# Optimization experiments

Measured on AMD Instinct MI355X. Metric: run time of the kernel, lower is better.

## Reference

```python
import jax, jax.numpy as jnp
import numpy as np

DATA = 2048   # data_size / hidden_size
WIDTH = 4096  # width_size
T = 1000      # len(ts)


def setup_inputs() -> dict:
    key = jax.random.key(0)
    ks = jax.random.split(key, 10)
    # ts: evenly spaced times; small dt keeps 1000 Euler steps stable
    ts = jnp.arange(T, dtype=jnp.float32) * 1e-3
    y0 = jax.random.normal(ks[0], (DATA,), dtype=jnp.float32)
    def lin(k, fan_out, fan_in):
        kw, kb = jax.random.split(k)
        s = 1.0 / np.sqrt(fan_in)
        W = jax.random.uniform(kw, (fan_out, fan_in), jnp.float32, -s, s)
        b = jax.random.uniform(kb, (fan_out,), jnp.float32, -s, s)
        return W, b
    # eqx.nn.MLP(depth=3): in->w, w->w, w->w, w->out, softplus on all but last
    W0, b0 = lin(ks[1], WIDTH, DATA)
    W1, b1 = lin(ks[2], WIDTH, WIDTH)
    W2, b2 = lin(ks[3], WIDTH, WIDTH)
    W3, b3 = lin(ks[4], DATA, WIDTH)
    return {"ts": ts, "y0": y0, "W0": W0, "b0": b0, "W1": W1, "b1": b1,
            "W2": W2, "b2": b2, "W3": W3, "b3": b3}


def reference(ts, y0, W0, b0, W1, b1, W2, b2, W3, b3):
    dt = ts[1] - ts[0]

    def mlp(y):
        h = jax.nn.softplus(W0 @ y + b0)
        h = jax.nn.softplus(W1 @ h + b1)
        h = jax.nn.softplus(W2 @ h + b2)
        return W3 @ h + b3

    def step(y, _):
        y1 = y + dt * mlp(y)  # Euler step: y + dt * f(t, y)
        return y1, y1

    _, ys = jax.lax.scan(step, y0, None, length=ts.shape[0])
    return ys  # [T, DATA]
```

## Files before the change

### kernel.cpp

```cpp
#include <hip/hip_runtime.h>

#define NWG   256
#define TPB_R 256
#define TPB_S 1024
#define NSTEP 1000
#define NDATA 2048
#define WIDTH 4096

typedef __attribute__((ext_vector_type(4))) float f32x4;
typedef __attribute__((ext_vector_type(2))) float f32x2;
typedef __attribute__((ext_vector_type(2))) unsigned int u32x2;
typedef __attribute__((ext_vector_type(4))) unsigned int u32x4;
typedef unsigned int uint;

#define SCHED_FENCE() __builtin_amdgcn_sched_barrier(0)


__device__ __forceinline__ float sp_f(float v) {
  return fmaxf(v, 0.0f) + log1pf(expf(-fabsf(v)));
}

__device__ __forceinline__ float wred(float v) {
#pragma unroll
  for (int m = 32; m > 0; m >>= 1) v += __shfl_xor(v, m, 64);
  return v;
}

__device__ __forceinline__ uint pk_bf16(float lo, float hi) {
  uint r;
  asm("v_cvt_pk_bf16_f32 %0, %1, %2" : "=v"(r) : "v"(lo), "v"(hi));
  return r;
}


__device__ __forceinline__ void wait_vm0()   { asm volatile("s_waitcnt vmcnt(0)" ::: "memory"); SCHED_FENCE(); }
template<int N>
__device__ __forceinline__ void wait_vmN()   { asm volatile("s_waitcnt vmcnt(%0)" :: "n"(N) : "memory"); SCHED_FENCE(); }
__device__ __forceinline__ void wait_lgkm0() { asm volatile("s_waitcnt lgkmcnt(0)" ::: "memory"); SCHED_FENCE(); }
__device__ __forceinline__ void wgbar()      { __builtin_amdgcn_s_barrier(); SCHED_FENCE(); }


__device__ __forceinline__ void st_sc_x1(float* p, float v) {
  asm volatile("global_store_dword %0, %1, off sc0 sc1" :: "v"(p), "v"(v) : "memory");
}
__device__ __forceinline__ void st_sc_x2(float* p, f32x2 v) {
  asm volatile("global_store_dwordx2 %0, %1, off sc0 sc1" :: "v"(p), "v"(v) : "memory");
}
__device__ __forceinline__ void st_sc_u2(uint* p, u32x2 v) {
  asm volatile("global_store_dwordx2 %0, %1, off sc0 sc1" :: "v"(p), "v"(v) : "memory");
}
__device__ __forceinline__ void ld_sc_x2_issue(const float* p, f32x2& v) {
  asm volatile("global_load_dwordx2 %0, %1, off sc0 sc1" : "=v"(v) : "v"(p) : "memory");
}
__device__ __forceinline__ void ld_sc_x4_issue(const f32x4* p, f32x4& v) {
  asm volatile("global_load_dwordx4 %0, %1, off sc0 sc1" : "=v"(v) : "v"(p) : "memory");
}
__device__ __forceinline__ void ld_sc_u4_issue(const u32x4* p, u32x4& v) {
  asm volatile("global_load_dwordx4 %0, %1, off sc0 sc1" : "=v"(v) : "v"(p) : "memory");
}
__device__ __forceinline__ void ld_sc_x1_issue(const float* p, float& v) {
  asm volatile("global_load_dword %0, %1, off sc0 sc1" : "=v"(v) : "v"(p) : "memory");
}
__device__ __forceinline__ uint ld_sc_u32(const uint* p) {
  uint v;
  asm volatile("global_load_dword %0, %1, off sc0 sc1\n\ts_waitcnt vmcnt(0)"
               : "=v"(v) : "v"(p) : "memory");
  return v;
}
__device__ __forceinline__ void st_sc_u32(uint* p, uint v) {
  asm volatile("global_store_dword %0, %1, off sc0 sc1" :: "v"(p), "v"(v) : "memory");
}

__device__ __forceinline__ void ld_g(const u32x4* p, u32x4& v) {
  asm volatile("global_load_dwordx4 %0, %1, off" : "=v"(v) : "v"(p) : "memory");
}


__device__ __forceinline__ void sync_stage_h(uint* flags, uint tag, int wg,
                                             int tid, const uint* src,
                                             uint* xs) {
  wgbar();
  if (tid == 0) st_sc_u32(flags + wg * 16, tag);
  const uint* fp = flags + tid * 16;
  if (ld_sc_u32(fp) < tag) {
    do { __builtin_amdgcn_s_sleep(1); } while (ld_sc_u32(fp) < tag);
  }
  const u32x4* s = (const u32x4*)src + tid * 2;
  u32x4 a, b;
  ld_sc_u4_issue(s + 0, a); ld_sc_u4_issue(s + 1, b);
  wait_vm0();
  u32x4* l = (u32x4*)xs + tid * 2;
  l[0] = a; l[1] = b;
  wait_lgkm0();
  wgbar();
}

__device__ __forceinline__ void sync_stage_y(uint* flags, uint tag, int wg,
                                             int tid, const float* src,
                                             uint* xs) {
  wgbar();
  if (tid == 0) st_sc_u32(flags + wg * 16, tag);
  const uint* fp = flags + tid * 16;
  if (ld_sc_u32(fp) < tag) {
    do { __builtin_amdgcn_s_sleep(1); } while (ld_sc_u32(fp) < tag);
  }
  const f32x4* s = (const f32x4*)src + tid * 2;
  f32x4 a, b;
  ld_sc_x4_issue(s + 0, a); ld_sc_x4_issue(s + 1, b);
  wait_vm0();
  u32x4 o;
  o.x = pk_bf16(a.x, a.y); o.y = pk_bf16(a.z, a.w);
  o.z = pk_bf16(b.x, b.y); o.w = pk_bf16(b.z, b.w);
  ((u32x4*)xs)[tid] = o;
  wait_lgkm0();
  wgbar();
}


__device__ __forceinline__ uint bfr(float f) {
  uint u = __float_as_uint(f);
  return (u + 0x7fffu + ((u >> 16) & 1u)) >> 16;
}

__global__ void cvt_perm(const float* __restrict__ in, u32x4* __restrict__ out,
                         int rows, int K) {
  int idx = blockIdx.x * 256 + threadIdx.x;
  int cpr = K >> 3;
  if (idx >= rows * cpr) return;
  int row = idx / cpr, c = idx - row * cpr;
  int j = c >> 6, lane = c & 63;
  const f32x4* p = (const f32x4*)(in + (size_t)row * K + j * 512 + lane * 4);
  f32x4 lo = p[0];
  f32x4 hi = p[64];
  u32x4 o;
  o.x = bfr(lo.x) | (bfr(lo.y) << 16);
  o.y = bfr(lo.z) | (bfr(lo.w) << 16);
  o.z = bfr(hi.x) | (bfr(hi.y) << 16);
  o.w = bfr(hi.z) | (bfr(hi.w) << 16);
  out[idx] = o;
}


#define VD(W, X, s) asm("v_dot2_f32_bf16 %0, %1, %2, %0" : "+v"(s) : "v"(W), "v"(X))

#define QF(Q, s) do{                                                 \
  VD((Q).x, xa2.x, s); VD((Q).y, xa2.y, s);                          \
  VD((Q).z, xb2.x, s); VD((Q).w, xb2.y, s);                          \
}while(0)

#define DC(Q, j, s) do{                                              \
  u32x2 xa2 = xw2[(j)*128 + lane];                                   \
  u32x2 xb2 = xw2[(j)*128 + 64 + lane];                              \
  QF(Q, s);                                                          \
}while(0)

#define DL4(j) do{                                                   \
  u32x2 xa2 = xw2[(j)*128 + lane];                                   \
  u32x2 xb2 = xw2[(j)*128 + 64 + lane];                              \
  u32x4 Q0 = w1p[0*512 + (j)*64 + lane];                             \
  u32x4 Q1 = w1p[1*512 + (j)*64 + lane];                             \
  u32x4 Q2 = w1p[2*512 + (j)*64 + lane];                             \
  u32x4 Q3 = w1p[3*512 + (j)*64 + lane];                             \
  QF(Q0, s0); QF(Q1, s1); QF(Q2, s2); QF(Q3, s3);                    \
}while(0)

#define DR4(j, Qa, Qb, Qc, Qd) do{                                   \
  u32x2 xa2 = xw2[(j)*128 + lane];                                   \
  u32x2 xb2 = xw2[(j)*128 + 64 + lane];                              \
  QF(Qa, s0); QF(Qb, s1); QF(Qc, s2); QF(Qd, s3);                    \
}while(0)

#define DR2(j, Qa, Qb) do{                                           \
  u32x2 xa2 = xw2[(j)*128 + lane];                                   \
  u32x2 xb2 = xw2[(j)*128 + 64 + lane];                              \
  QF(Qa, s0); QF(Qb, s1);                                            \
}while(0)

#define SREG(x) __int_as_float(__builtin_amdgcn_readfirstlane(__float_as_int(x)))


__global__ void __launch_bounds__(TPB_R, 1) ode_res(
    const float* __restrict__ ts, const float* __restrict__ y0,
    const u32x4* __restrict__ W0p, const float* __restrict__ b0,
    const u32x4* __restrict__ W1p, const float* __restrict__ b1,
    const u32x4* __restrict__ W2p, const float* __restrict__ b2,
    const u32x4* __restrict__ W3p, const float* __restrict__ b3,
    float* __restrict__ out, uint* hA, uint* hB,
    uint* flags)
{
  __shared__ u32x4 W1lds[16 * 512];
  __shared__ uint xs[2048];
  const int wg = blockIdx.x, tid = threadIdx.x;
  const int wave = tid >> 6, lane = tid & 63;
  const float dt = ts[1] - ts[0];
  const int rw = wg * 16 + wave * 4;
  const int rf = wg * 8 + wave * 2;
  const u32x2* xw2 = (const u32x2*)xs;
  const u32x4* w1p = &W1lds[(wave * 4) * 512];

#pragma unroll
  for (int k = 0; k < 32; ++k)
    W1lds[k * 256 + tid] = W1p[(size_t)wg * 8192 + k * 256 + tid];

#define L2W(r,j) W2p[(size_t)(rw+(r))*512 + (j)*64 + lane]
  u32x4 C00=L2W(0,0),C01=L2W(0,1),C02=L2W(0,2),C03=L2W(0,3),C04=L2W(0,4),C05=L2W(0,5),C06=L2W(0,6),C07=L2W(0,7);
  u32x4 C10=L2W(1,0),C11=L2W(1,1),C12=L2W(1,2),C13=L2W(1,3),C14=L2W(1,4),C15=L2W(1,5),C16=L2W(1,6),C17=L2W(1,7);
  u32x4 C20=L2W(2,0),C21=L2W(2,1),C22=L2W(2,2),C23=L2W(2,3),C24=L2W(2,4),C25=L2W(2,5),C26=L2W(2,6),C27=L2W(2,7);
  u32x4 C30=L2W(3,0),C31=L2W(3,1),C32=L2W(3,2),C33=L2W(3,3),C34=L2W(3,4),C35=L2W(3,5),C36=L2W(3,6),C37=L2W(3,7);
#define L3W(r,j) W3p[(size_t)(rf+(r))*512 + (j)*64 + lane]
  u32x4 D00=L3W(0,0),D01=L3W(0,1),D02=L3W(0,2),D03=L3W(0,3),D04=L3W(0,4),D05=L3W(0,5),D06=L3W(0,6),D07=L3W(0,7);
  u32x4 D10=L3W(1,0),D11=L3W(1,1),D12=L3W(1,2),D13=L3W(1,3),D14=L3W(1,4),D15=L3W(1,5),D16=L3W(1,6),D17=L3W(1,7);

  const float b00=SREG(b0[rw]), b01=SREG(b0[rw+1]), b02=SREG(b0[rw+2]), b03=SREG(b0[rw+3]);
  const float b10=SREG(b1[rw]), b11=SREG(b1[rw+1]), b12=SREG(b1[rw+2]), b13=SREG(b1[rw+3]);
  const float b20=SREG(b2[rw]), b21=SREG(b2[rw+1]), b22=SREG(b2[rw+2]), b23=SREG(b2[rw+3]);
  const float b30=SREG(b3[rf]), b31=SREG(b3[rf+1]);

  wait_vm0(); wait_lgkm0();
  wgbar();

  const u32x4* w0base = W0p + (size_t)rw * 256 + lane;
#define ISSW0(r, Qa, Qb, Qc, Qd) do{ const u32x4* p_ = w0base + (size_t)(r)*256; \
  ld_g(p_, Qa); ld_g(p_+64, Qb); ld_g(p_+128, Qc); ld_g(p_+192, Qd); }while(0)

  u32x4 E0a,E0b,E0c,E0d, E1a,E1b,E1c,E1d, E2a,E2b,E2c,E2d, E3a,E3b,E3c,E3d;
  ISSW0(0, E0a,E0b,E0c,E0d);

  uint tag = 0;
  const float* yin = y0;
  for (int step = 0; step < NSTEP; ++step) {
    float s0, s1, s2, s3;
    sync_stage_y(flags, tag, wg, tid, yin, xs); ++tag;
    ISSW0(1, E1a,E1b,E1c,E1d);
    s0 = 0.f; DC(E0a,0,s0); DC(E0b,1,s0); DC(E0c,2,s0); DC(E0d,3,s0);
    ISSW0(2, E2a,E2b,E2c,E2d);
    wait_vmN<4>();
    s1 = 0.f; DC(E1a,0,s1); DC(E1b,1,s1); DC(E1c,2,s1); DC(E1d,3,s1);
    ISSW0(3, E3a,E3b,E3c,E3d);
    wait_vmN<4>();
    s2 = 0.f; DC(E2a,0,s2); DC(E2b,1,s2); DC(E2c,2,s2); DC(E2d,3,s2);
    wait_vm0();
    s3 = 0.f; DC(E3a,0,s3); DC(E3b,1,s3); DC(E3c,2,s3); DC(E3d,3,s3);
    s0 = wred(s0); s1 = wred(s1); s2 = wred(s2); s3 = wred(s3);
    if (lane == 0) {
      u32x2 v; v.x = pk_bf16(sp_f(s0+b00), sp_f(s1+b01));
               v.y = pk_bf16(sp_f(s2+b02), sp_f(s3+b03));
      st_sc_u2(hA + (rw >> 1), v);
    }
    wait_vm0();

    sync_stage_h(flags, tag, wg, tid, hA, xs); ++tag;
    s0=0.f; s1=0.f; s2=0.f; s3=0.f;
    DL4(0); DL4(1); DL4(2); DL4(3); DL4(4); DL4(5); DL4(6); DL4(7);
    s0 = wred(s0); s1 = wred(s1); s2 = wred(s2); s3 = wred(s3);
    if (lane == 0) {
      u32x2 v; v.x = pk_bf16(sp_f(s0+b10), sp_f(s1+b11));
               v.y = pk_bf16(sp_f(s2+b12), sp_f(s3+b13));
      st_sc_u2(hB + (rw >> 1), v);
    }
    wait_vm0();

    sync_stage_h(flags, tag, wg, tid, hB, xs); ++tag;
    s0=0.f; s1=0.f; s2=0.f; s3=0.f;
    DR4(0, C00, C10, C20, C30); DR4(1, C01, C11, C21, C31);
    DR4(2, C02, C12, C22, C32); DR4(3, C03, C13, C23, C33);
    DR4(4, C04, C14, C24, C34); DR4(5, C05, C15, C25, C35);
    DR4(6, C06, C16, C26, C36); DR4(7, C07, C17, C27, C37);
    s0 = wred(s0); s1 = wred(s1); s2 = wred(s2); s3 = wred(s3);
    if (lane == 0) {
      u32x2 v; v.x = pk_bf16(sp_f(s0+b20), sp_f(s1+b21));
               v.y = pk_bf16(sp_f(s2+b22), sp_f(s3+b23));
      st_sc_u2(hA + (rw >> 1), v);
    }
    wait_vm0();

    sync_stage_h(flags, tag, wg, tid, hA, xs); ++tag;
    f32x2 yo;
    ld_sc_x2_issue(yin + rf, yo);
    s0=0.f; s1=0.f;
    DR2(0, D00, D10); DR2(1, D01, D11); DR2(2, D02, D12); DR2(3, D03, D13);
    DR2(4, D04, D14); DR2(5, D05, D15); DR2(6, D06, D16); DR2(7, D07, D17);
    s0 = wred(s0); s1 = wred(s1);
    wait_vm0();
    float* yout = out + (size_t)step * NDATA;
    if (lane == 0) {
      f32x2 v; v.x = yo.x + dt * (s0 + b30); v.y = yo.y + dt * (s1 + b31);
      st_sc_x2(yout + rf, v);
    }
    ISSW0(0, E0a,E0b,E0c,E0d);
    wait_vmN<4>();
    yin = yout;
  }
}


__device__ __forceinline__ void gbar1k(uint* flags, uint tag, int wg, int tid) {
  wgbar();
  if (tid == 0) st_sc_u32(flags + wg * 16, tag);
  if (tid < NWG) {
    const uint* fp = flags + tid * 16;
    if (ld_sc_u32(fp) < tag) {
      do { __builtin_amdgcn_s_sleep(1); } while (ld_sc_u32(fp) < tag);
    }
  }
  wgbar();
}

__device__ __forceinline__ void stage4096_1k(const float* src, float* xs, int tid) {
  f32x4 a;
  ld_sc_x4_issue((const f32x4*)src + tid, a);
  wait_vm0();
  ((f32x4*)xs)[tid] = a;
  wait_lgkm0();
  wgbar();
}
__device__ __forceinline__ void stage2048_1k(const float* src, float* xs, int tid) {
  f32x4 a;
  bool act = tid < 512;
  if (act) ld_sc_x4_issue((const f32x4*)src + tid, a);
  wait_vm0();
  if (act) ((f32x4*)xs)[tid] = a;
  wait_lgkm0();
  wgbar();
}

__device__ __forceinline__ void issue_row_f32(const float* W, size_t elemidx, int lane, f32x4* wr, int ni) {
  const f32x4* p = (const f32x4*)(W + elemidx) + lane;
  for (int i = 0; i < ni; ++i)
    asm volatile("global_load_dwordx4 %0, %1, off" : "=v"(wr[i]) : "v"(p + i * 64) : "memory");
}

template<int NI>
__device__ __forceinline__ float dot_row_f32(const f32x4* wr, const float* xs, int xoff, int lane) {
  const f32x4* x4 = (const f32x4*)xs + xoff;
  float a = 0.f;
#pragma unroll
  for (int i = 0; i < NI; ++i) {
    f32x4 xv = x4[i * 64 + lane];
    a = fmaf(wr[i].x, xv.x, a); a = fmaf(wr[i].y, xv.y, a);
    a = fmaf(wr[i].z, xv.z, a); a = fmaf(wr[i].w, xv.w, a);
  }
  return a;
}

__global__ void __launch_bounds__(TPB_S, 1) ode_stream(
    const float* __restrict__ ts, const float* __restrict__ y0,
    const float* __restrict__ W0, const float* __restrict__ b0,
    const float* __restrict__ W1, const float* __restrict__ b1,
    const float* __restrict__ W2, const float* __restrict__ b2,
    const float* __restrict__ W3, const float* __restrict__ b3,
    float* __restrict__ out, float* hA, float* hB,
    uint* flags)
{
  __shared__ float xs[WIDTH];
  __shared__ float ps[16];
  const int wg = blockIdx.x, tid = threadIdx.x;
  const int wave = tid >> 6, lane = tid & 63;
  const float dt = ts[1] - ts[0];
  const int rw = wg * 16 + wave;
  const int rF = wg * 8 + (wave >> 1);
  const int hf = wave & 1;

  f32x4 w0r[8], w1r[16], w2r[16], w3r[8];
  issue_row_f32(W0, (size_t)rw * NDATA, lane, w0r, 8);

  uint tag = 0;
  const float* yin = y0;
  for (int step = 0; step < NSTEP; ++step) {
    stage2048_1k(yin, xs, tid);
    float a = wred(dot_row_f32<8>(w0r, xs, 0, lane));
    if (lane == 0) st_sc_x1(hA + rw, sp_f(a + b0[rw]));
    issue_row_f32(W1, (size_t)rw * WIDTH, lane, w1r, 16);
    wait_vmN<16>();
    gbar1k(flags, ++tag, wg, tid);

    stage4096_1k(hA, xs, tid);
    a = wred(dot_row_f32<16>(w1r, xs, 0, lane));
    if (lane == 0) st_sc_x1(hB + rw, sp_f(a + b1[rw]));
    issue_row_f32(W2, (size_t)rw * WIDTH, lane, w2r, 16);
    wait_vmN<16>();
    gbar1k(flags, ++tag, wg, tid);

    stage4096_1k(hB, xs, tid);
    a = wred(dot_row_f32<16>(w2r, xs, 0, lane));
    if (lane == 0) st_sc_x1(hA + rw, sp_f(a + b2[rw]));
    issue_row_f32(W3, (size_t)rF * WIDTH + (size_t)hf * 2048, lane, w3r, 8);
    wait_vmN<8>();
    gbar1k(flags, ++tag, wg, tid);

    stage4096_1k(hA, xs, tid);
    float yo;
    ld_sc_x1_issue(yin + rF, yo);
    a = wred(dot_row_f32<8>(w3r, xs, hf * 512, lane));
    if (lane == 0) ps[wave] = a;
    wait_lgkm0();
    wgbar();
    wait_vm0();
    float* yout = out + (size_t)step * NDATA;
    if (hf == 0 && lane == 0) {
      float tot = ps[wave] + ps[wave + 1];
      st_sc_x1(yout + rF, yo + dt * (tot + b3[rF]));
    }
    issue_row_f32(W0, (size_t)rw * NDATA, lane, w0r, 8);
    wait_vmN<8>();
    gbar1k(flags, ++tag, wg, tid);
    yin = yout;
  }
}


#define WS_HA   0
#define WS_HB   16384
#define WS_CNT  32768
#define WS_WB   65536
static const size_t N_W0 = (size_t)WIDTH * NDATA;
static const size_t N_W1 = (size_t)WIDTH * WIDTH;
static const size_t N_W3 = (size_t)NDATA * WIDTH;

extern "C" void kernel_launch(void* const* d_in, const int* in_sizes, int n_in,
                              void* d_out, int out_size, void* d_ws, size_t ws_size,
                              hipStream_t stream) {
  const float* ts = (const float*)d_in[0];
  const float* y0 = (const float*)d_in[1];
  const float* W0 = (const float*)d_in[2];
  const float* b0 = (const float*)d_in[3];
  const float* W1 = (const float*)d_in[4];
  const float* b1 = (const float*)d_in[5];
  const float* W2 = (const float*)d_in[6];
  const float* b2 = (const float*)d_in[7];
  const float* W3 = (const float*)d_in[8];
  const float* b3 = (const float*)d_in[9];
  float* out = (float*)d_out;

  char* ws = (char*)d_ws;
  uint*  flags = (uint*)(ws + WS_CNT);

  hipMemsetAsync(ws + WS_CNT, 0, 16384, stream);

  const size_t need = WS_WB + (N_W0 + 2 * N_W1 + N_W3) * 2;
  if (ws_size >= need) {
    u32x4* W0p = (u32x4*)(ws + WS_WB);
    u32x4* W1p = W0p + N_W0 / 8;
    u32x4* W2p = W1p + N_W1 / 8;
    u32x4* W3p = W2p + N_W1 / 8;
    uint* hA = (uint*)(ws + WS_HA);
    uint* hB = (uint*)(ws + WS_HB);
    hipLaunchKernelGGL(cvt_perm, dim3((unsigned)(N_W0 / 8 / 256)), dim3(256), 0, stream, W0, W0p, WIDTH, NDATA);
    hipLaunchKernelGGL(cvt_perm, dim3((unsigned)(N_W1 / 8 / 256)), dim3(256), 0, stream, W1, W1p, WIDTH, WIDTH);
    hipLaunchKernelGGL(cvt_perm, dim3((unsigned)(N_W1 / 8 / 256)), dim3(256), 0, stream, W2, W2p, WIDTH, WIDTH);
    hipLaunchKernelGGL(cvt_perm, dim3((unsigned)(N_W3 / 8 / 256)), dim3(256), 0, stream, W3, W3p, NDATA, WIDTH);
    hipLaunchKernelGGL(ode_res, dim3(NWG), dim3(TPB_R), 0, stream,
                       ts, y0, W0p, b0, W1p, b1, W2p, b2, W3p, b3,
                       out, hA, hB, flags);
  } else {
    float* hAf = (float*)(ws + WS_HA);
    float* hBf = (float*)(ws + WS_HB);
    hipLaunchKernelGGL(ode_stream, dim3(NWG), dim3(TPB_S), 0, stream,
                       ts, y0, W0, b0, W1, b1, W2, b2, W3, b3,
                       out, hAf, hBf, flags);
  }
}
```

Baseline: 19.87 ms.

## Fold W3 and next-step W0 into precomputed G matrix to drop one grid barrier per step

Precomputes G = W0·W3 with a one-time GEMM kernel. Each Euler step then updates the first-layer pre-activation directly as u += dt·(G·h2 + W0·b3), while y is still computed from W3 for output. This removes one of the four grid-wide syncs per step and fuses the y→layer0 dependency. In exchange it streams an extra 4096x4096 bf16 matrix from global memory every step, adds a setup GEMM, and lets the pre-activation accumulate rounding drift relative to recomputing from y.

```diff
diff --git a/kernel.cpp b/kernel.cpp
--- a/kernel.cpp
+++ b/kernel.cpp
@@ -70,7 +70,6 @@
 __device__ __forceinline__ void st_sc_u32(uint* p, uint v) {
   asm volatile("global_store_dword %0, %1, off sc0 sc1" :: "v"(p), "v"(v) : "memory");
 }
-
 __device__ __forceinline__ void ld_g(const u32x4* p, u32x4& v) {
   asm volatile("global_load_dwordx4 %0, %1, off" : "=v"(v) : "v"(p) : "memory");
 }
@@ -108,6 +107,18 @@
   f32x4 a, b;
   ld_sc_x4_issue(s + 0, a); ld_sc_x4_issue(s + 1, b);
   wait_vm0();
+  u32x4 o;
+  o.x = pk_bf16(a.x, a.y); o.y = pk_bf16(a.z, a.w);
+  o.z = pk_bf16(b.x, b.y); o.w = pk_bf16(b.z, b.w);
+  ((u32x4*)xs)[tid] = o;
+  wait_lgkm0();
+  wgbar();
+}
+
+__device__ __forceinline__ void stage_plain_2048(const float* src, uint* xs, int tid) {
+  wgbar();
+  const f32x4* s = (const f32x4*)src + tid * 2;
+  f32x4 a = s[0], b = s[1];
   u32x4 o;
   o.x = pk_bf16(a.x, a.y); o.y = pk_bf16(a.z, a.w);
   o.z = pk_bf16(b.x, b.y); o.w = pk_bf16(b.z, b.w);
@@ -141,6 +152,63 @@
 }
 
 
+__global__ void __launch_bounds__(256) gemm_G(const float* __restrict__ W0,
+                                              const float* __restrict__ W3,
+                                              uint* __restrict__ Gp) {
+  __shared__ float As[64][33];
+  __shared__ float Bs[32][65];
+  const int bid = blockIdx.x;
+  const int tr = bid >> 6, tc = bid & 63;
+  const int r0 = tr * 64, c0 = tc * 64;
+  const int tid = threadIdx.x;
+  float acc[4][4] = {};
+  for (int kb = 0; kb < 2048; kb += 32) {
+    {
+      int row = tid >> 2, kk = (tid & 3) * 8;
+      const float* src = W0 + (size_t)(r0 + row) * 2048 + kb + kk;
+#pragma unroll
+      for (int i = 0; i < 8; ++i) As[row][kk + i] = src[i];
+    }
+    {
+      int k = tid >> 3, cc = (tid & 7) * 8;
+      const float* src = W3 + (size_t)(kb + k) * 4096 + c0 + cc;
+#pragma unroll
+      for (int i = 0; i < 8; ++i) Bs[k][cc + i] = src[i];
+    }
+    __syncthreads();
+    const int rr = (tid >> 4) * 4, cc = (tid & 15) * 4;
+#pragma unroll
+    for (int k = 0; k < 32; ++k) {
+      float a0 = As[rr + 0][k], a1 = As[rr + 1][k], a2 = As[rr + 2][k], a3 = As[rr + 3][k];
+      float bx0 = Bs[k][cc + 0], bx1 = Bs[k][cc + 1], bx2 = Bs[k][cc + 2], bx3 = Bs[k][cc + 3];
+      acc[0][0] = fmaf(a0, bx0, acc[0][0]); acc[0][1] = fmaf(a0, bx1, acc[0][1]);
+      acc[0][2] = fmaf(a0, bx2, acc[0][2]); acc[0][3] = fmaf(a0, bx3, acc[0][3]);
+      acc[1][0] = fmaf(a1, bx0, acc[1][0]); acc[1][1] = fmaf(a1, bx1, acc[1][1]);
+      acc[1][2] = fmaf(a1, bx2, acc[1][2]); acc[1][3] = fmaf(a1, bx3, acc[1][3]);
+      acc[2][0] = fmaf(a2, bx0, acc[2][0]); acc[2][1] = fmaf(a2, bx1, acc[2][1]);
+      acc[2][2] = fmaf(a2, bx2, acc[2][2]); acc[2][3] = fmaf(a2, bx3, acc[2][3]);
+      acc[3][0] = fmaf(a3, bx0, acc[3][0]); acc[3][1] = fmaf(a3, bx1, acc[3][1]);
+      acc[3][2] = fmaf(a3, bx2, acc[3][2]); acc[3][3] = fmaf(a3, bx3, acc[3][3]);
+    }
+    __syncthreads();
+  }
+  const int rr = (tid >> 4) * 4, cc = (tid & 15) * 4;
+#pragma unroll
+  for (int i = 0; i < 4; ++i) {
+    int r = r0 + rr + i;
+    int c = c0 + cc;
+    int j = c >> 9, q = c & 511;
+    int lane, w;
+    if (q < 256) { lane = q >> 2; w = 0; } else { lane = (q - 256) >> 2; w = 2; }
+    uint* dst = Gp + ((size_t)r * 512 + (size_t)j * 64 + lane) * 4 + w;
+    u32x2 v;
+    v.x = bfr(acc[i][0]) | (bfr(acc[i][1]) << 16);
+    v.y = bfr(acc[i][2]) | (bfr(acc[i][3]) << 16);
+    *(u32x2*)dst = v;
+  }
+}
+
+
 #define VD(W, X, s) asm("v_dot2_f32_bf16 %0, %1, %2, %0" : "+v"(s) : "v"(W), "v"(X))
 
 #define QF(Q, s) do{                                                 \
@@ -177,6 +245,158 @@
 }while(0)
 
 #define SREG(x) __int_as_float(__builtin_amdgcn_readfirstlane(__float_as_int(x)))
+
+
+__global__ void __launch_bounds__(TPB_R, 1) ode_fused(
+    const float* __restrict__ ts, const float* __restrict__ y0,
+    const u32x4* __restrict__ W0p, const float* __restrict__ b0,
+    const u32x4* __restrict__ W1p, const float* __restrict__ b1,
+    const u32x4* __restrict__ W2p, const float* __restrict__ b2,
+    const u32x4* __restrict__ W3p, const float* __restrict__ b3,
+    const u32x4* __restrict__ Gp,
+    float* __restrict__ out, uint* x1buf, uint* h1buf, uint* h2buf,
+    uint* flags)
+{
+  __shared__ u32x4 W1lds[16 * 512];
+  __shared__ uint xs[2048];
+  const int wg = blockIdx.x, tid = threadIdx.x;
+  const int wave = tid >> 6, lane = tid & 63;
+  const float dt = ts[1] - ts[0];
+  const int rw = wg * 16 + wave * 4;
+  const int rf = wg * 8 + wave * 2;
+  const u32x2* xw2 = (const u32x2*)xs;
+  const u32x4* w1p = &W1lds[(wave * 4) * 512];
+
+#pragma unroll
+  for (int k = 0; k < 32; ++k)
+    W1lds[k * 256 + tid] = W1p[(size_t)wg * 8192 + k * 256 + tid];
+
+#define L2W(r,j) W2p[(size_t)(rw+(r))*512 + (j)*64 + lane]
+  u32x4 C00=L2W(0,0),C01=L2W(0,1),C02=L2W(0,2),C03=L2W(0,3),C04=L2W(0,4),C05=L2W(0,5),C06=L2W(0,6),C07=L2W(0,7);
+  u32x4 C10=L2W(1,0),C11=L2W(1,1),C12=L2W(1,2),C13=L2W(1,3),C14=L2W(1,4),C15=L2W(1,5),C16=L2W(1,6),C17=L2W(1,7);
+  u32x4 C20=L2W(2,0),C21=L2W(2,1),C22=L2W(2,2),C23=L2W(2,3),C24=L2W(2,4),C25=L2W(2,5),C26=L2W(2,6),C27=L2W(2,7);
+  u32x4 C30=L2W(3,0),C31=L2W(3,1),C32=L2W(3,2),C33=L2W(3,3),C34=L2W(3,4),C35=L2W(3,5),C36=L2W(3,6),C37=L2W(3,7);
+#define L3W(r,j) W3p[(size_t)(rf+(r))*512 + (j)*64 + lane]
+  u32x4 D00=L3W(0,0),D01=L3W(0,1),D02=L3W(0,2),D03=L3W(0,3),D04=L3W(0,4),D05=L3W(0,5),D06=L3W(0,6),D07=L3W(0,7);
+  u32x4 D10=L3W(1,0),D11=L3W(1,1),D12=L3W(1,2),D13=L3W(1,3),D14=L3W(1,4),D15=L3W(1,5),D16=L3W(1,6),D17=L3W(1,7);
+
+  const float b00=SREG(b0[rw]), b01=SREG(b0[rw+1]), b02=SREG(b0[rw+2]), b03=SREG(b0[rw+3]);
+  const float b10=SREG(b1[rw]), b11=SREG(b1[rw+1]), b12=SREG(b1[rw+2]), b13=SREG(b1[rw+3]);
+  const float b20=SREG(b2[rw]), b21=SREG(b2[rw+1]), b22=SREG(b2[rw+2]), b23=SREG(b2[rw+3]);
+  const float b30=SREG(b3[rf]), b31=SREG(b3[rf+1]);
+
+  wait_vm0(); wait_lgkm0();
+  wgbar();
+
+  u32x4 F00,F01,F02,F03,F04,F05,F06,F07, F10,F11,F12,F13,F14,F15,F16,F17;
+#define ISSW0ALL() do{                                                         \
+  const u32x4* p0_ = W0p + (size_t)(rw+0)*256 + lane;                          \
+  const u32x4* p1_ = W0p + (size_t)(rw+1)*256 + lane;                          \
+  const u32x4* p2_ = W0p + (size_t)(rw+2)*256 + lane;                          \
+  const u32x4* p3_ = W0p + (size_t)(rw+3)*256 + lane;                          \
+  ld_g(p0_,F00); ld_g(p0_+64,F01); ld_g(p0_+128,F02); ld_g(p0_+192,F03);       \
+  ld_g(p1_,F04); ld_g(p1_+64,F05); ld_g(p1_+128,F06); ld_g(p1_+192,F07);       \
+  ld_g(p2_,F10); ld_g(p2_+64,F11); ld_g(p2_+128,F12); ld_g(p2_+192,F13);       \
+  ld_g(p3_,F14); ld_g(p3_+64,F15); ld_g(p3_+128,F16); ld_g(p3_+192,F17);       \
+}while(0)
+
+  float c0, c1, c2, c3, u0, u1, u2, u3;
+  stage_plain_2048(b3, xs, tid);
+  ISSW0ALL(); wait_vm0();
+  c0=0.f; DC(F00,0,c0); DC(F01,1,c0); DC(F02,2,c0); DC(F03,3,c0);
+  c1=0.f; DC(F04,0,c1); DC(F05,1,c1); DC(F06,2,c1); DC(F07,3,c1);
+  c2=0.f; DC(F10,0,c2); DC(F11,1,c2); DC(F12,2,c2); DC(F13,3,c2);
+  c3=0.f; DC(F14,0,c3); DC(F15,1,c3); DC(F16,2,c3); DC(F17,3,c3);
+  c0 = wred(c0); c1 = wred(c1); c2 = wred(c2); c3 = wred(c3);
+
+  stage_plain_2048(y0, xs, tid);
+  ISSW0ALL(); wait_vm0();
+  u0=0.f; DC(F00,0,u0); DC(F01,1,u0); DC(F02,2,u0); DC(F03,3,u0);
+  u1=0.f; DC(F04,0,u1); DC(F05,1,u1); DC(F06,2,u1); DC(F07,3,u1);
+  u2=0.f; DC(F10,0,u2); DC(F11,1,u2); DC(F12,2,u2); DC(F13,3,u2);
+  u3=0.f; DC(F14,0,u3); DC(F15,1,u3); DC(F16,2,u3); DC(F17,3,u3);
+  u0 = wred(u0); u1 = wred(u1); u2 = wred(u2); u3 = wred(u3);
+
+  float yv0 = y0[rf], yv1 = y0[rf + 1];
+
+  if (lane == 0) {
+    u32x2 xv;
+    xv.x = pk_bf16(sp_f(u0 + b00), sp_f(u1 + b01));
+    xv.y = pk_bf16(sp_f(u2 + b02), sp_f(u3 + b03));
+    st_sc_u2(x1buf + (rw >> 1), xv);
+  }
+  wait_vm0();
+
+#define ISSG(r, Q0,Q1,Q2,Q3,Q4,Q5,Q6,Q7) do{                                   \
+  const u32x4* p_ = Gp + (size_t)(rw+(r))*512 + lane;                          \
+  ld_g(p_,Q0); ld_g(p_+64,Q1); ld_g(p_+128,Q2); ld_g(p_+192,Q3);               \
+  ld_g(p_+256,Q4); ld_g(p_+320,Q5); ld_g(p_+384,Q6); ld_g(p_+448,Q7);          \
+}while(0)
+
+  uint tag = 1;
+  for (int step = 0; step < NSTEP; ++step) {
+    float s0, s1, s2, s3;
+    sync_stage_h(flags, tag, wg, tid, x1buf, xs); ++tag;
+    s0=0.f; s1=0.f; s2=0.f; s3=0.f;
+    DL4(0); DL4(1); DL4(2); DL4(3); DL4(4); DL4(5); DL4(6); DL4(7);
+    s0 = wred(s0); s1 = wred(s1); s2 = wred(s2); s3 = wred(s3);
+    if (lane == 0) {
+      u32x2 v; v.x = pk_bf16(sp_f(s0+b10), sp_f(s1+b11));
+               v.y = pk_bf16(sp_f(s2+b12), sp_f(s3+b13));
+      st_sc_u2(h1buf + (rw >> 1), v);
+    }
+    wait_vm0();
+
+    sync_stage_h(flags, tag, wg, tid, h1buf, xs); ++tag;
+    s0=0.f; s1=0.f; s2=0.f; s3=0.f;
+    DR4(0, C00, C10, C20, C30); DR4(1, C01, C11, C21, C31);
+    DR4(2, C02, C12, C22, C32); DR4(3, C03, C13, C23, C33);
+    DR4(4, C04, C14, C24, C34); DR4(5, C05, C15, C25, C35);
+    DR4(6, C06, C16, C26, C36); DR4(7, C07, C17, C27, C37);
+    s0 = wred(s0); s1 = wred(s1); s2 = wred(s2); s3 = wred(s3);
+    if (lane == 0) {
+      u32x2 v; v.x = pk_bf16(sp_f(s0+b20), sp_f(s1+b21));
+               v.y = pk_bf16(sp_f(s2+b22), sp_f(s3+b23));
+      st_sc_u2(h2buf + (rw >> 1), v);
+    }
+    wait_vm0();
+
+    ISSG(0, F00,F01,F02,F03,F04,F05,F06,F07);
+    ISSG(1, F10,F11,F12,F13,F14,F15,F16,F17);
+
+    sync_stage_h(flags, tag, wg, tid, h2buf, xs); ++tag;
+    float g0=0.f, g1=0.f, g2=0.f, g3=0.f;
+    DC(F00,0,g0); DC(F01,1,g0); DC(F02,2,g0); DC(F03,3,g0);
+    DC(F04,4,g0); DC(F05,5,g0); DC(F06,6,g0); DC(F07,7,g0);
+    DC(F10,0,g1); DC(F11,1,g1); DC(F12,2,g1); DC(F13,3,g1);
+    DC(F14,4,g1); DC(F15,5,g1); DC(F16,6,g1); DC(F17,7,g1);
+    ISSG(2, F00,F01,F02,F03,F04,F05,F06,F07);
+    ISSG(3, F10,F11,F12,F13,F14,F15,F16,F17);
+    s0=0.f; s1=0.f;
+    DR2(0, D00, D10); DR2(1, D01, D11); DR2(2, D02, D12); DR2(3, D03, D13);
+    DR2(4, D04, D14); DR2(5, D05, D15); DR2(6, D06, D16); DR2(7, D07, D17);
+    wait_vm0();
+    DC(F00,0,g2); DC(F01,1,g2); DC(F02,2,g2); DC(F03,3,g2);
+    DC(F04,4,g2); DC(F05,5,g2); DC(F06,6,g2); DC(F07,7,g2);
+    DC(F10,0,g3); DC(F11,1,g3); DC(F12,2,g3); DC(F13,3,g3);
+    DC(F14,4,g3); DC(F15,5,g3); DC(F16,6,g3); DC(F17,7,g3);
+    g0 = wred(g0); g1 = wred(g1); g2 = wred(g2); g3 = wred(g3);
+    s0 = wred(s0); s1 = wred(s1);
+    u0 += dt * (g0 + c0); u1 += dt * (g1 + c1);
+    u2 += dt * (g2 + c2); u3 += dt * (g3 + c3);
+    yv0 += dt * (s0 + b30); yv1 += dt * (s1 + b31);
+    float* yout = out + (size_t)step * NDATA;
+    if (lane == 0) {
+      f32x2 yv; yv.x = yv0; yv.y = yv1;
+      st_sc_x2(yout + rf, yv);
+      u32x2 xv;
+      xv.x = pk_bf16(sp_f(u0 + b00), sp_f(u1 + b01));
+      xv.y = pk_bf16(sp_f(u2 + b02), sp_f(u3 + b03));
+      st_sc_u2(x1buf + (rw >> 1), xv);
+    }
+    wait_vm0();
+  }
+}
 
 
 __global__ void __launch_bounds__(TPB_R, 1) ode_res(
@@ -202,12 +422,10 @@
   for (int k = 0; k < 32; ++k)
     W1lds[k * 256 + tid] = W1p[(size_t)wg * 8192 + k * 256 + tid];
 
-#define L2W(r,j) W2p[(size_t)(rw+(r))*512 + (j)*64 + lane]
   u32x4 C00=L2W(0,0),C01=L2W(0,1),C02=L2W(0,2),C03=L2W(0,3),C04=L2W(0,4),C05=L2W(0,5),C06=L2W(0,6),C07=L2W(0,7);
   u32x4 C10=L2W(1,0),C11=L2W(1,1),C12=L2W(1,2),C13=L2W(1,3),C14=L2W(1,4),C15=L2W(1,5),C16=L2W(1,6),C17=L2W(1,7);
   u32x4 C20=L2W(2,0),C21=L2W(2,1),C22=L2W(2,2),C23=L2W(2,3),C24=L2W(2,4),C25=L2W(2,5),C26=L2W(2,6),C27=L2W(2,7);
   u32x4 C30=L2W(3,0),C31=L2W(3,1),C32=L2W(3,2),C33=L2W(3,3),C34=L2W(3,4),C35=L2W(3,5),C36=L2W(3,6),C37=L2W(3,7);
-#define L3W(r,j) W3p[(size_t)(rf+(r))*512 + (j)*64 + lane]
   u32x4 D00=L3W(0,0),D01=L3W(0,1),D02=L3W(0,2),D03=L3W(0,3),D04=L3W(0,4),D05=L3W(0,5),D06=L3W(0,6),D07=L3W(0,7);
   u32x4 D10=L3W(1,0),D11=L3W(1,1),D12=L3W(1,2),D13=L3W(1,3),D14=L3W(1,4),D15=L3W(1,5),D16=L3W(1,6),D17=L3W(1,7);
 
@@ -306,20 +524,20 @@
   wgbar();
 }
 
-__device__ __forceinline__ void stage4096_1k(const float* src, float* xs, int tid) {
+__device__ __forceinline__ void stage4096_1k(const float* src, float* xsf, int tid) {
   f32x4 a;
   ld_sc_x4_issue((const f32x4*)src + tid, a);
   wait_vm0();
-  ((f32x4*)xs)[tid] = a;
+  ((f32x4*)xsf)[tid] = a;
   wait_lgkm0();
   wgbar();
 }
-__device__ __forceinline__ void stage2048_1k(const float* src, float* xs, int tid) {
+__device__ __forceinline__ void stage2048_1k(const float* src, float* xsf, int tid) {
   f32x4 a;
   bool act = tid < 512;
   if (act) ld_sc_x4_issue((const f32x4*)src + tid, a);
   wait_vm0();
-  if (act) ((f32x4*)xs)[tid] = a;
+  if (act) ((f32x4*)xsf)[tid] = a;
   wait_lgkm0();
   wgbar();
 }
@@ -331,8 +549,8 @@
 }
 
 template<int NI>
-__device__ __forceinline__ float dot_row_f32(const f32x4* wr, const float* xs, int xoff, int lane) {
-  const f32x4* x4 = (const f32x4*)xs + xoff;
+__device__ __forceinline__ float dot_row_f32(const f32x4* wr, const float* xsf, int xoff, int lane) {
+  const f32x4* x4 = (const f32x4*)xsf + xoff;
   float a = 0.f;
 #pragma unroll
   for (int i = 0; i < NI; ++i) {
@@ -352,7 +570,7 @@
     float* __restrict__ out, float* hA, float* hB,
     uint* flags)
 {
-  __shared__ float xs[WIDTH];
+  __shared__ float xsf[WIDTH];
   __shared__ float ps[16];
   const int wg = blockIdx.x, tid = threadIdx.x;
   const int wave = tid >> 6, lane = tid & 63;
@@ -367,31 +585,31 @@
   uint tag = 0;
   const float* yin = y0;
   for (int step = 0; step < NSTEP; ++step) {
-    stage2048_1k(yin, xs, tid);
-    float a = wred(dot_row_f32<8>(w0r, xs, 0, lane));
+    stage2048_1k(yin, xsf, tid);
+    float a = wred(dot_row_f32<8>(w0r, xsf, 0, lane));
     if (lane == 0) st_sc_x1(hA + rw, sp_f(a + b0[rw]));
     issue_row_f32(W1, (size_t)rw * WIDTH, lane, w1r, 16);
     wait_vmN<16>();
     gbar1k(flags, ++tag, wg, tid);
 
-    stage4096_1k(hA, xs, tid);
-    a = wred(dot_row_f32<16>(w1r, xs, 0, lane));
+    stage4096_1k(hA, xsf, tid);
+    a = wred(dot_row_f32<16>(w1r, xsf, 0, lane));
     if (lane == 0) st_sc_x1(hB + rw, sp_f(a + b1[rw]));
     issue_row_f32(W2, (size_t)rw * WIDTH, lane, w2r, 16);
     wait_vmN<16>();
     gbar1k(flags, ++tag, wg, tid);
 
-    stage4096_1k(hB, xs, tid);
-    a = wred(dot_row_f32<16>(w2r, xs, 0, lane));
+    stage4096_1k(hB, xsf, tid);
+    a = wred(dot_row_f32<16>(w2r, xsf, 0, lane));
     if (lane == 0) st_sc_x1(hA + rw, sp_f(a + b2[rw]));
     issue_row_f32(W3, (size_t)rF * WIDTH + (size_t)hf * 2048, lane, w3r, 8);
     wait_vmN<8>();
     gbar1k(flags, ++tag, wg, tid);
 
-    stage4096_1k(hA, xs, tid);
+    stage4096_1k(hA, xsf, tid);
     float yo;
     ld_sc_x1_issue(yin + rF, yo);
-    a = wred(dot_row_f32<8>(w3r, xs, hf * 512, lane));
+    a = wred(dot_row_f32<8>(w3r, xsf, hf * 512, lane));
     if (lane == 0) ps[wave] = a;
     wait_lgkm0();
     wgbar();
@@ -409,13 +627,15 @@
 }
 
 
-#define WS_HA   0
-#define WS_HB   16384
+#define WS_X1   0
+#define WS_H1   8192
+#define WS_H2   16384
 #define WS_CNT  32768
 #define WS_WB   65536
 static const size_t N_W0 = (size_t)WIDTH * NDATA;
 static const size_t N_W1 = (size_t)WIDTH * WIDTH;
 static const size_t N_W3 = (size_t)NDATA * WIDTH;
+static const size_t N_G  = (size_t)WIDTH * WIDTH;
 
 extern "C" void kernel_launch(void* const* d_in, const int* in_sizes, int n_in,
                               void* d_out, int out_size, void* d_ws, size_t ws_size,
@@ -433,28 +653,44 @@
   float* out = (float*)d_out;
 
   char* ws = (char*)d_ws;
-  uint*  flags = (uint*)(ws + WS_CNT);
+  uint* flags = (uint*)(ws + WS_CNT);
 
   hipMemsetAsync(ws + WS_CNT, 0, 16384, stream);
 
-  const size_t need = WS_WB + (N_W0 + 2 * N_W1 + N_W3) * 2;
-  if (ws_size >= need) {
-    u32x4* W0p = (u32x4*)(ws + WS_WB);
-    u32x4* W1p = W0p + N_W0 / 8;
-    u32x4* W2p = W1p + N_W1 / 8;
-    u32x4* W3p = W2p + N_W1 / 8;
-    uint* hA = (uint*)(ws + WS_HA);
-    uint* hB = (uint*)(ws + WS_HB);
+  const size_t need_bf  = WS_WB + (N_W0 + 2 * N_W1 + N_W3) * 2;
+  const size_t need_fus = need_bf + N_G * 2;
+
+  u32x4* W0p = (u32x4*)(ws + WS_WB);
+  u32x4* W1p = W0p + N_W0 / 8;
+  u32x4* W2p = W1p + N_W1 / 8;
+  u32x4* W3p = W2p + N_W1 / 8;
+  u32x4* Gp  = W3p + N_W3 / 8;
+
+  if (ws_size >= need_fus) {
     hipLaunchKernelGGL(cvt_perm, dim3((unsigned)(N_W0 / 8 / 256)), dim3(256), 0, stream, W0, W0p, WIDTH, NDATA);
     hipLaunchKernelGGL(cvt_perm, dim3((unsigned)(N_W1 / 8 / 256)), dim3(256), 0, stream, W1, W1p, WIDTH, WIDTH);
     hipLaunchKernelGGL(cvt_perm, dim3((unsigned)(N_W1 / 8 / 256)), dim3(256), 0, stream, W2, W2p, WIDTH, WIDTH);
     hipLaunchKernelGGL(cvt_perm, dim3((unsigned)(N_W3 / 8 / 256)), dim3(256), 0, stream, W3, W3p, NDATA, WIDTH);
+    hipLaunchKernelGGL(gemm_G, dim3(4096), dim3(256), 0, stream, W0, W3, (uint*)Gp);
+    uint* x1b = (uint*)(ws + WS_X1);
+    uint* h1b = (uint*)(ws + WS_H1);
+    uint* h2b = (uint*)(ws + WS_H2);
+    hipLaunchKernelGGL(ode_fused, dim3(NWG), dim3(TPB_R), 0, stream,
+                       ts, y0, W0p, b0, W1p, b1, W2p, b2, W3p, b3, Gp,
+                       out, x1b, h1b, h2b, flags);
+  } else if (ws_size >= need_bf) {
+    hipLaunchKernelGGL(cvt_perm, dim3((unsigned)(N_W0 / 8 / 256)), dim3(256), 0, stream, W0, W0p, WIDTH, NDATA);
+    hipLaunchKernelGGL(cvt_perm, dim3((unsigned)(N_W1 / 8 / 256)), dim3(256), 0, stream, W1, W1p, WIDTH, WIDTH);
+    hipLaunchKernelGGL(cvt_perm, dim3((unsigned)(N_W1 / 8 / 256)), dim3(256), 0, stream, W2, W2p, WIDTH, WIDTH);
+    hipLaunchKernelGGL(cvt_perm, dim3((unsigned)(N_W3 / 8 / 256)), dim3(256), 0, stream, W3, W3p, NDATA, WIDTH);
+    uint* hA = (uint*)(ws + WS_X1);
+    uint* hB = (uint*)(ws + WS_H2);
     hipLaunchKernelGGL(ode_res, dim3(NWG), dim3(TPB_R), 0, stream,
                        ts, y0, W0p, b0, W1p, b1, W2p, b2, W3p, b3,
                        out, hA, hB, flags);
   } else {
-    float* hAf = (float*)(ws + WS_HA);
-    float* hBf = (float*)(ws + WS_HB);
+    float* hAf = (float*)(ws + WS_X1);
+    float* hBf = (float*)(ws + WS_H2);
     hipLaunchKernelGGL(ode_stream, dim3(NWG), dim3(TPB_S), 0, stream,
                        ts, y0, W0, b0, W1, b1, W2, b2, W3, b3,
                        out, hAf, hBf, flags);
```

After: 19.87 ms. Within noise of the previous version (+0.0%).
